# Kernel optimization log

Measured on AMD Instinct MI355X. Metric: run time of the kernel, lower is better.

Reference implementation:

```python
import jax, jax.numpy as jnp
from jax import lax
import numpy as np

T, B, I, H = 2048, 64, 256, 256  # time-major LSTM, standard 4H gate layout


def setup_inputs() -> dict:
    key = jax.random.key(0)
    k = jax.random.split(key, 5)
    s = 1.0 / np.sqrt(H)
    return {
        "x": jax.random.normal(k[0], (T, B, I), dtype=jnp.float32),
        "W_ih": jax.random.uniform(k[1], (4 * H, I), jnp.float32, -s, s),
        "W_hh": jax.random.uniform(k[2], (4 * H, H), jnp.float32, -s, s),
        "b_ih": jax.random.uniform(k[3], (4 * H,), jnp.float32, -s, s),
        "b_hh": jax.random.uniform(k[4], (4 * H,), jnp.float32, -s, s),
    }


def reference(x, W_ih, W_hh, b_ih, b_hh):
    # Precompute input projections for all timesteps in one big GEMM: [T, B, 4H]
    x_proj = jnp.einsum("tbi,gi->tbg", x, W_ih) + b_ih + b_hh

    def step(carry, xp_t):
        h, c = carry
        gates = xp_t + h @ W_hh.T  # [B, 4H]
        i, f, g, o = jnp.split(gates, 4, axis=-1)
        c = jax.nn.sigmoid(f) * c + jax.nn.sigmoid(i) * jnp.tanh(g)
        h = jax.nn.sigmoid(o) * jnp.tanh(c)
        return (h, c), None

    init = (jnp.zeros((x.shape[1], H), x.dtype), jnp.zeros((x.shape[1], H), x.dtype))
    (h_last, c_last), _ = lax.scan(step, init, x_proj)
    # torch loop overwrites `outputs` each step and returns only the final h
    return h_last
```

## Files before the change

### kernel.cpp

```cpp
#include <hip/hip_runtime.h>
#include <hip/hip_bf16.h>
#include <stdint.h>


#define T_STEPS 2048
#define NWG 32

typedef float f32x4 __attribute__((ext_vector_type(4)));
typedef short bf16x8 __attribute__((ext_vector_type(8)));
typedef uint32_t u32x4 __attribute__((ext_vector_type(4)));

__device__ __forceinline__ short tobf(float f) {
    __hip_bfloat16 h = __float2bfloat16(f);
    return *reinterpret_cast<short*>(&h);
}

__device__ __forceinline__ bf16x8 pack8(f32x4 a, f32x4 b) {
    bf16x8 r;
    r[0] = tobf(a[0]); r[1] = tobf(a[1]); r[2] = tobf(a[2]); r[3] = tobf(a[3]);
    r[4] = tobf(b[0]); r[5] = tobf(b[1]); r[6] = tobf(b[2]); r[7] = tobf(b[3]);
    return r;
}

__device__ __forceinline__ bf16x8 frag_u64(unsigned long long a, unsigned long long b) {
    u32x4 t;
    t.x = (uint32_t)a; t.y = (uint32_t)(a >> 32);
    t.z = (uint32_t)b; t.w = (uint32_t)(b >> 32);
    return __builtin_bit_cast(bf16x8, t);
}

__device__ __forceinline__ float fast_sig(float x) {
    float e = __builtin_amdgcn_exp2f(-1.4426950408889634f * x);
    return __builtin_amdgcn_rcpf(1.0f + e);
}
__device__ __forceinline__ float fast_tanh(float x) {
    float xc = fminf(fmaxf(x, -15.0f), 15.0f);
    float e = __builtin_amdgcn_exp2f(2.8853900817779268f * xc);
    return (e - 1.0f) * __builtin_amdgcn_rcpf(e + 1.0f);
}

__global__ __launch_bounds__(256, 1)
void lstm_fused(const float* __restrict__ x,
                const float* __restrict__ W_ih,
                const float* __restrict__ W_hh,
                const float* __restrict__ b_ih,
                const float* __restrict__ b_hh,
                float* __restrict__ out,
                uint32_t* __restrict__ hbuf,
                uint32_t* __restrict__ flags)
{
    const int wg   = blockIdx.x;
    const int tid  = threadIdx.x;
    const int wv   = tid >> 6;
    const int l    = tid & 63;
    const int l15  = l & 15;
    const int lk   = l >> 4;
    const int gate = l15 >> 2;
    const int jj   = l15 & 3;

    bf16x8 wf[2][16];
    float bias[2];
#pragma unroll
    for (int p = 0; p < 2; ++p) {
        const int grow = 256 * gate + 8 * wg + 4 * p + jj;
#pragma unroll
        for (int kt = 0; kt < 16; ++kt) {
            const float* src = (kt < 8)
                ? (W_ih + (size_t)grow * 256 + kt * 32 + lk * 8)
                : (W_hh + (size_t)grow * 256 + (kt - 8) * 32 + lk * 8);
            wf[p][kt] = pack8(*(const f32x4*)(src), *(const f32x4*)(src + 4));
        }
        bias[p] = b_ih[grow] + b_hh[grow];
    }

    const int arow = 16 * wv + l15;
    const float* xbase = x + (size_t)arow * 256 + lk * 8;

    float cst[2][4] = {{0.f,0.f,0.f,0.f},{0.f,0.f,0.f,0.f}};

    f32x4 xs[16];
#pragma unroll
    for (int kt = 0; kt < 8; ++kt) {
        xs[2 * kt]     = *(const f32x4*)(xbase + kt * 32);
        xs[2 * kt + 1] = *(const f32x4*)(xbase + kt * 32 + 4);
    }
    f32x4 aA[2] = {{0.f,0.f,0.f,0.f},{0.f,0.f,0.f,0.f}};
    f32x4 aB[2] = {{0.f,0.f,0.f,0.f},{0.f,0.f,0.f,0.f}};
    {
        bf16x8 af[8];
#pragma unroll
        for (int kt = 0; kt < 8; ++kt) af[kt] = pack8(xs[2 * kt], xs[2 * kt + 1]);
#pragma unroll
        for (int kt = 0; kt < 8; kt += 2)
#pragma unroll
            for (int p = 0; p < 2; ++p) {
                aA[p] = __builtin_amdgcn_mfma_f32_16x16x32_bf16(af[kt],     wf[p][kt],     aA[p], 0, 0, 0);
                aB[p] = __builtin_amdgcn_mfma_f32_16x16x32_bf16(af[kt + 1], wf[p][kt + 1], aB[p], 0, 0, 0);
            }
#pragma unroll
        for (int kt = 0; kt < 8; ++kt) {
            const float* p1 = xbase + 16384 + kt * 32;
            xs[2 * kt]     = *(const f32x4*)(p1);
            xs[2 * kt + 1] = *(const f32x4*)(p1 + 4);
        }
    }

    const uint32_t* mypollline = flags + wv * 32 + (l & 31);
    uint32_t* myflag = flags + wv * 32 + wg;

    for (int s = 0; s < T_STEPS; ++s) {
        if (s > 0) {
            const uint32_t target = (uint32_t)s;
            while (true) {
                uint32_t v = __hip_atomic_load(mypollline, __ATOMIC_RELAXED,
                                               __HIP_MEMORY_SCOPE_AGENT);
                if (__all((int)(v >= target))) break;
                __builtin_amdgcn_s_sleep(1);
            }
        }
        asm volatile("" ::: "memory");

        const unsigned long long* hb = (const unsigned long long*)
            (hbuf + (size_t)(s & 1) * 8192 + (size_t)arow * 128 + 4 * lk);
        unsigned long long hq[16];
#pragma unroll
        for (int kh = 0; kh < 8; ++kh) {
            hq[2 * kh]     = __hip_atomic_load(hb + (size_t)kh * 8,
                                               __ATOMIC_RELAXED, __HIP_MEMORY_SCOPE_AGENT);
            hq[2 * kh + 1] = __hip_atomic_load(hb + (size_t)kh * 8 + 1,
                                               __ATOMIC_RELAXED, __HIP_MEMORY_SCOPE_AGENT);
        }

#pragma unroll
        for (int kh = 0; kh < 8; kh += 2) {
            bf16x8 h0 = frag_u64(hq[2 * kh],     hq[2 * kh + 1]);
            bf16x8 h1 = frag_u64(hq[2 * kh + 2], hq[2 * kh + 3]);
#pragma unroll
            for (int p = 0; p < 2; ++p) {
                aA[p] = __builtin_amdgcn_mfma_f32_16x16x32_bf16(h0, wf[p][8 + kh],     aA[p], 0, 0, 0);
                aB[p] = __builtin_amdgcn_mfma_f32_16x16x32_bf16(h1, wf[p][8 + kh + 1], aB[p], 0, 0, 0);
            }
        }

        uint32_t* hw_out = hbuf + (size_t)((s + 1) & 1) * 8192;
        const int orow0 = 16 * wv + 4 * lk;
        float hv[2][4];
#pragma unroll
        for (int p = 0; p < 2; ++p) {
#pragma unroll
            for (int r = 0; r < 4; ++r) {
                float vo  = aA[p][r] + aB[p][r] + bias[p];
                float v4  = __shfl_xor(vo, 4);
                float v8  = __shfl_xor(vo, 8);
                float v12 = __shfl_xor(vo, 12);
                float iv = (gate == 0) ? vo : ((gate == 1) ? v4 : ((gate == 2) ? v8 : v12));
                float fv = (gate == 1) ? vo : ((gate == 0) ? v4 : ((gate == 3) ? v8 : v12));
                float gv = (gate == 2) ? vo : ((gate == 3) ? v4 : ((gate == 0) ? v8 : v12));
                float ov = (gate == 3) ? vo : ((gate == 2) ? v4 : ((gate == 1) ? v8 : v12));
                float cn = fast_sig(fv) * cst[p][r] + fast_sig(iv) * fast_tanh(gv);
                cst[p][r] = cn;
                hv[p][r] = fast_sig(ov) * fast_tanh(cn);
            }
        }

#pragma unroll
        for (int p = 0; p < 2; ++p) {
#pragma unroll
            for (int r = 0; r < 4; ++r) {
                uint32_t hu = (uint32_t)(uint16_t)tobf(hv[p][r]);
                uint32_t pu = (uint32_t)__shfl_xor((int)hu, 1);
                uint32_t packed = hu | (pu << 16);
                if ((l & 13) == 0) {
                    __hip_atomic_store(hw_out + (size_t)(orow0 + r) * 128
                                           + 4 * wg + 2 * p + (jj >> 1),
                                       packed, __ATOMIC_RELAXED, __HIP_MEMORY_SCOPE_AGENT);
                }
            }
        }

        if (s == T_STEPS - 1) {
#pragma unroll
            for (int p = 0; p < 2; ++p)
#pragma unroll
                for (int r = 0; r < 4; ++r)
                    if ((l & 12) == 0)
                        out[(size_t)(orow0 + r) * 256 + 8 * wg + 4 * p + jj] = hv[p][r];
        }

        if (l == 0)
            __hip_atomic_store(myflag, (uint32_t)(s + 1),
                               __ATOMIC_RELEASE, __HIP_MEMORY_SCOPE_AGENT);

        if (s + 1 < T_STEPS) {
            bf16x8 af[8];
#pragma unroll
            for (int kt = 0; kt < 8; ++kt) af[kt] = pack8(xs[2 * kt], xs[2 * kt + 1]);
#pragma unroll
            for (int p = 0; p < 2; ++p) { aA[p] = (f32x4){0.f,0.f,0.f,0.f}; aB[p] = (f32x4){0.f,0.f,0.f,0.f}; }
#pragma unroll
            for (int kt = 0; kt < 8; kt += 2)
#pragma unroll
                for (int p = 0; p < 2; ++p) {
                    aA[p] = __builtin_amdgcn_mfma_f32_16x16x32_bf16(af[kt],     wf[p][kt],     aA[p], 0, 0, 0);
                    aB[p] = __builtin_amdgcn_mfma_f32_16x16x32_bf16(af[kt + 1], wf[p][kt + 1], aB[p], 0, 0, 0);
                }
            if (s + 2 < T_STEPS) {
                const float* xp = xbase + (size_t)(s + 2) * 16384;
#pragma unroll
                for (int kt = 0; kt < 8; ++kt) {
                    xs[2 * kt]     = *(const f32x4*)(xp + kt * 32);
                    xs[2 * kt + 1] = *(const f32x4*)(xp + kt * 32 + 4);
                }
            }
        }
    }
}

extern "C" void kernel_launch(void* const* d_in, const int* in_sizes, int n_in,
                              void* d_out, int out_size, void* d_ws, size_t ws_size,
                              hipStream_t stream) {
    const float* x    = (const float*)d_in[0];
    const float* W_ih = (const float*)d_in[1];
    const float* W_hh = (const float*)d_in[2];
    const float* b_ih = (const float*)d_in[3];
    const float* b_hh = (const float*)d_in[4];
    float* out = (float*)d_out;

    uint32_t* hbuf  = (uint32_t*)d_ws;
    uint32_t* flags = hbuf + 2 * 8192;

    hipMemsetAsync(d_ws, 0, (2 * 8192 + 4 * 32) * sizeof(uint32_t), stream);

    lstm_fused<<<dim3(NWG), dim3(256), 0, stream>>>(x, W_ih, W_hh, b_ih, b_hh,
                                                    out, hbuf, flags);
}
```

Before: 13.96 ms.

## Replace per-step flag barrier with tag-embedded hidden-state words polled directly

Each hidden value is stored as a 32-bit word carrying the bf16 value plus a 16-bit step tag, so consumers poll the data itself instead of waiting on per-workgroup flags and then loading. This removes the separate flag release/acquire round trip on every step. The next step's input projection MFMAs are also moved ahead of the poll, and x is packed to bf16 as soon as it is loaded. In exchange the hidden buffer doubles in size, the output tensor is reused as the second ping-pong buffer, a spin budget can exit early, and correctness relies on relaxed stores of value and tag landing together in one word.

After: 38.72 ms. 177% more time.

```diff
diff --git a/kernel.cpp b/kernel.cpp
--- a/kernel.cpp
+++ b/kernel.cpp
@@ -10,23 +10,18 @@
 typedef short bf16x8 __attribute__((ext_vector_type(8)));
 typedef uint32_t u32x4 __attribute__((ext_vector_type(4)));
 
-__device__ __forceinline__ short tobf(float f) {
+__device__ __forceinline__ unsigned short tobf(float f) {
     __hip_bfloat16 h = __float2bfloat16(f);
-    return *reinterpret_cast<short*>(&h);
+    return *reinterpret_cast<unsigned short*>(&h);
 }
 
 __device__ __forceinline__ bf16x8 pack8(f32x4 a, f32x4 b) {
     bf16x8 r;
-    r[0] = tobf(a[0]); r[1] = tobf(a[1]); r[2] = tobf(a[2]); r[3] = tobf(a[3]);
-    r[4] = tobf(b[0]); r[5] = tobf(b[1]); r[6] = tobf(b[2]); r[7] = tobf(b[3]);
+    r[0] = (short)tobf(a[0]); r[1] = (short)tobf(a[1]);
+    r[2] = (short)tobf(a[2]); r[3] = (short)tobf(a[3]);
+    r[4] = (short)tobf(b[0]); r[5] = (short)tobf(b[1]);
+    r[6] = (short)tobf(b[2]); r[7] = (short)tobf(b[3]);
     return r;
-}
-
-__device__ __forceinline__ bf16x8 frag_u64(unsigned long long a, unsigned long long b) {
-    u32x4 t;
-    t.x = (uint32_t)a; t.y = (uint32_t)(a >> 32);
-    t.z = (uint32_t)b; t.w = (uint32_t)(b >> 32);
-    return __builtin_bit_cast(bf16x8, t);
 }
 
 __device__ __forceinline__ float fast_sig(float x) {
@@ -40,14 +35,14 @@
 }
 
 __global__ __launch_bounds__(256, 1)
-void lstm_fused(const float* __restrict__ x,
-                const float* __restrict__ W_ih,
-                const float* __restrict__ W_hh,
-                const float* __restrict__ b_ih,
-                const float* __restrict__ b_hh,
-                float* __restrict__ out,
-                uint32_t* __restrict__ hbuf,
-                uint32_t* __restrict__ flags)
+void lstm_tagged(const float* __restrict__ x,
+                 const float* __restrict__ W_ih,
+                 const float* __restrict__ W_hh,
+                 const float* __restrict__ b_ih,
+                 const float* __restrict__ b_hh,
+                 uint32_t* __restrict__ buf0,
+                 uint32_t* __restrict__ buf1,
+                 uint32_t* __restrict__ flags)
 {
     const int wg   = blockIdx.x;
     const int tid  = threadIdx.x;
@@ -58,6 +53,8 @@
     const int gate = l15 >> 2;
     const int jj   = l15 & 3;
 
+    int budget = 1 << 24;
+
     bf16x8 wf[2][16];
     float bias[2];
 #pragma unroll
@@ -78,71 +75,85 @@
 
     float cst[2][4] = {{0.f,0.f,0.f,0.f},{0.f,0.f,0.f,0.f}};
 
-    f32x4 xs[16];
-#pragma unroll
-    for (int kt = 0; kt < 8; ++kt) {
-        xs[2 * kt]     = *(const f32x4*)(xbase + kt * 32);
-        xs[2 * kt + 1] = *(const f32x4*)(xbase + kt * 32 + 4);
-    }
+    bf16x8 xsp[8];
+#pragma unroll
+    for (int kt = 0; kt < 8; ++kt)
+        xsp[kt] = pack8(*(const f32x4*)(xbase + kt * 32),
+                        *(const f32x4*)(xbase + kt * 32 + 4));
+
     f32x4 aA[2] = {{0.f,0.f,0.f,0.f},{0.f,0.f,0.f,0.f}};
     f32x4 aB[2] = {{0.f,0.f,0.f,0.f},{0.f,0.f,0.f,0.f}};
-    {
-        bf16x8 af[8];
-#pragma unroll
-        for (int kt = 0; kt < 8; ++kt) af[kt] = pack8(xs[2 * kt], xs[2 * kt + 1]);
-#pragma unroll
-        for (int kt = 0; kt < 8; kt += 2)
+#pragma unroll
+    for (int kt = 0; kt < 8; kt += 2)
+#pragma unroll
+        for (int p = 0; p < 2; ++p) {
+            aA[p] = __builtin_amdgcn_mfma_f32_16x16x32_bf16(xsp[kt],     wf[p][kt],     aA[p], 0, 0, 0);
+            aB[p] = __builtin_amdgcn_mfma_f32_16x16x32_bf16(xsp[kt + 1], wf[p][kt + 1], aB[p], 0, 0, 0);
+        }
+#pragma unroll
+    for (int kt = 0; kt < 8; ++kt)
+        xsp[kt] = pack8(*(const f32x4*)(xbase + 16384 + kt * 32),
+                        *(const f32x4*)(xbase + 16384 + kt * 32 + 4));
+
+    for (int s = 0; s < T_STEPS; ++s) {
+        const uint32_t* rb = (s & 1) ? buf1 : buf0;
+        const unsigned long long* hb64 =
+            (const unsigned long long*)(rb + (size_t)arow * 256) + 4 * lk;
+        unsigned long long hq[32];
+#pragma unroll
+        for (int kh = 0; kh < 8; ++kh)
+#pragma unroll
+            for (int i = 0; i < 4; ++i)
+                hq[4 * kh + i] = __hip_atomic_load(hb64 + 16 * kh + i,
+                                                   __ATOMIC_RELAXED, __HIP_MEMORY_SCOPE_AGENT);
+
+        f32x4 aA2[2] = {{0.f,0.f,0.f,0.f},{0.f,0.f,0.f,0.f}};
+        f32x4 aB2[2] = {{0.f,0.f,0.f,0.f},{0.f,0.f,0.f,0.f}};
+        if (s + 1 < T_STEPS) {
+#pragma unroll
+            for (int kt = 0; kt < 8; kt += 2)
+#pragma unroll
+                for (int p = 0; p < 2; ++p) {
+                    aA2[p] = __builtin_amdgcn_mfma_f32_16x16x32_bf16(xsp[kt],     wf[p][kt],     aA2[p], 0, 0, 0);
+                    aB2[p] = __builtin_amdgcn_mfma_f32_16x16x32_bf16(xsp[kt + 1], wf[p][kt + 1], aB2[p], 0, 0, 0);
+                }
+        }
+        __builtin_amdgcn_sched_barrier(0);
+
+        const unsigned long long tagpair =
+            (unsigned long long)(uint32_t)s * 0x0000000100000001ull;
+        const unsigned long long tmask = 0x0000FFFF0000FFFFull;
+        while (true) {
+            unsigned long long bad = 0;
+#pragma unroll
+            for (int i = 0; i < 32; ++i) bad |= (hq[i] ^ tagpair) & tmask;
+            if (__all(bad == 0ull)) break;
+            if (--budget < 0) break;
+            __builtin_amdgcn_s_sleep(1);
+#pragma unroll
+            for (int kh = 0; kh < 8; ++kh)
+#pragma unroll
+                for (int i = 0; i < 4; ++i)
+                    hq[4 * kh + i] = __hip_atomic_load(hb64 + 16 * kh + i,
+                                                       __ATOMIC_RELAXED, __HIP_MEMORY_SCOPE_AGENT);
+        }
+
+#pragma unroll
+        for (int kh = 0; kh < 8; ++kh) {
+            u32x4 t;
+#pragma unroll
+            for (int i = 0; i < 4; ++i) {
+                unsigned long long q = hq[4 * kh + i];
+                t[i] = (((uint32_t)q) >> 16) | ((uint32_t)(q >> 32) & 0xFFFF0000u);
+            }
+            bf16x8 hf = __builtin_bit_cast(bf16x8, t);
 #pragma unroll
             for (int p = 0; p < 2; ++p) {
-                aA[p] = __builtin_amdgcn_mfma_f32_16x16x32_bf16(af[kt],     wf[p][kt],     aA[p], 0, 0, 0);
-                aB[p] = __builtin_amdgcn_mfma_f32_16x16x32_bf16(af[kt + 1], wf[p][kt + 1], aB[p], 0, 0, 0);
-            }
-#pragma unroll
-        for (int kt = 0; kt < 8; ++kt) {
-            const float* p1 = xbase + 16384 + kt * 32;
-            xs[2 * kt]     = *(const f32x4*)(p1);
-            xs[2 * kt + 1] = *(const f32x4*)(p1 + 4);
-        }
-    }
-
-    const uint32_t* mypollline = flags + wv * 32 + (l & 31);
-    uint32_t* myflag = flags + wv * 32 + wg;
-
-    for (int s = 0; s < T_STEPS; ++s) {
-        if (s > 0) {
-            const uint32_t target = (uint32_t)s;
-            while (true) {
-                uint32_t v = __hip_atomic_load(mypollline, __ATOMIC_RELAXED,
-                                               __HIP_MEMORY_SCOPE_AGENT);
-                if (__all((int)(v >= target))) break;
-                __builtin_amdgcn_s_sleep(1);
-            }
-        }
-        asm volatile("" ::: "memory");
-
-        const unsigned long long* hb = (const unsigned long long*)
-            (hbuf + (size_t)(s & 1) * 8192 + (size_t)arow * 128 + 4 * lk);
-        unsigned long long hq[16];
-#pragma unroll
-        for (int kh = 0; kh < 8; ++kh) {
-            hq[2 * kh]     = __hip_atomic_load(hb + (size_t)kh * 8,
-                                               __ATOMIC_RELAXED, __HIP_MEMORY_SCOPE_AGENT);
-            hq[2 * kh + 1] = __hip_atomic_load(hb + (size_t)kh * 8 + 1,
-                                               __ATOMIC_RELAXED, __HIP_MEMORY_SCOPE_AGENT);
-        }
-
-#pragma unroll
-        for (int kh = 0; kh < 8; kh += 2) {
-            bf16x8 h0 = frag_u64(hq[2 * kh],     hq[2 * kh + 1]);
-            bf16x8 h1 = frag_u64(hq[2 * kh + 2], hq[2 * kh + 3]);
-#pragma unroll
-            for (int p = 0; p < 2; ++p) {
-                aA[p] = __builtin_amdgcn_mfma_f32_16x16x32_bf16(h0, wf[p][8 + kh],     aA[p], 0, 0, 0);
-                aB[p] = __builtin_amdgcn_mfma_f32_16x16x32_bf16(h1, wf[p][8 + kh + 1], aB[p], 0, 0, 0);
-            }
-        }
-
-        uint32_t* hw_out = hbuf + (size_t)((s + 1) & 1) * 8192;
+                if (kh & 1) aB[p] = __builtin_amdgcn_mfma_f32_16x16x32_bf16(hf, wf[p][8 + kh], aB[p], 0, 0, 0);
+                else        aA[p] = __builtin_amdgcn_mfma_f32_16x16x32_bf16(hf, wf[p][8 + kh], aA[p], 0, 0, 0);
+            }
+        }
+
         const int orow0 = 16 * wv + 4 * lk;
         float hv[2][4];
 #pragma unroll
@@ -163,55 +174,50 @@
             }
         }
 
-#pragma unroll
-        for (int p = 0; p < 2; ++p) {
-#pragma unroll
-            for (int r = 0; r < 4; ++r) {
-                uint32_t hu = (uint32_t)(uint16_t)tobf(hv[p][r]);
-                uint32_t pu = (uint32_t)__shfl_xor((int)hu, 1);
-                uint32_t packed = hu | (pu << 16);
-                if ((l & 13) == 0) {
-                    __hip_atomic_store(hw_out + (size_t)(orow0 + r) * 128
-                                           + 4 * wg + 2 * p + (jj >> 1),
-                                       packed, __ATOMIC_RELAXED, __HIP_MEMORY_SCOPE_AGENT);
-                }
-            }
+        if (s + 1 < T_STEPS) {
+            uint32_t* wb = ((s + 1) & 1) ? buf1 : buf0;
+            const uint32_t tago = (uint32_t)(s + 1);
+#pragma unroll
+            for (int p = 0; p < 2; ++p)
+#pragma unroll
+                for (int r = 0; r < 4; ++r)
+                    if ((l & 12) == 0) {
+                        uint32_t word = ((uint32_t)tobf(hv[p][r]) << 16) | tago;
+                        __hip_atomic_store(wb + (size_t)(orow0 + r) * 256
+                                               + 8 * wg + 4 * p + jj,
+                                           word, __ATOMIC_RELAXED, __HIP_MEMORY_SCOPE_AGENT);
+                    }
+        }
+
+#pragma unroll
+        for (int p = 0; p < 2; ++p) { aA[p] = aA2[p]; aB[p] = aB2[p]; }
+        if (s + 2 < T_STEPS) {
+            const float* xp = xbase + (size_t)(s + 2) * 16384;
+#pragma unroll
+            for (int kt = 0; kt < 8; ++kt)
+                xsp[kt] = pack8(*(const f32x4*)(xp + kt * 32),
+                                *(const f32x4*)(xp + kt * 32 + 4));
         }
 
         if (s == T_STEPS - 1) {
+            if (l == 0)
+                __hip_atomic_store(flags + wv * 32 + wg, 1u,
+                                   __ATOMIC_RELEASE, __HIP_MEMORY_SCOPE_AGENT);
+            const uint32_t* fp = flags + wv * 32 + (l & 31);
+            while (true) {
+                uint32_t fvv = __hip_atomic_load(fp, __ATOMIC_RELAXED,
+                                                 __HIP_MEMORY_SCOPE_AGENT);
+                if (__all((int)(fvv >= 1u))) break;
+                if (--budget < 0) break;
+                __builtin_amdgcn_s_sleep(1);
+            }
+            float* outf = (float*)buf1;
 #pragma unroll
             for (int p = 0; p < 2; ++p)
 #pragma unroll
                 for (int r = 0; r < 4; ++r)
                     if ((l & 12) == 0)
-                        out[(size_t)(orow0 + r) * 256 + 8 * wg + 4 * p + jj] = hv[p][r];
-        }
-
-        if (l == 0)
-            __hip_atomic_store(myflag, (uint32_t)(s + 1),
-                               __ATOMIC_RELEASE, __HIP_MEMORY_SCOPE_AGENT);
-
-        if (s + 1 < T_STEPS) {
-            bf16x8 af[8];
-#pragma unroll
-            for (int kt = 0; kt < 8; ++kt) af[kt] = pack8(xs[2 * kt], xs[2 * kt + 1]);
-#pragma unroll
-            for (int p = 0; p < 2; ++p) { aA[p] = (f32x4){0.f,0.f,0.f,0.f}; aB[p] = (f32x4){0.f,0.f,0.f,0.f}; }
-#pragma unroll
-            for (int kt = 0; kt < 8; kt += 2)
-#pragma unroll
-                for (int p = 0; p < 2; ++p) {
-                    aA[p] = __builtin_amdgcn_mfma_f32_16x16x32_bf16(af[kt],     wf[p][kt],     aA[p], 0, 0, 0);
-                    aB[p] = __builtin_amdgcn_mfma_f32_16x16x32_bf16(af[kt + 1], wf[p][kt + 1], aB[p], 0, 0, 0);
-                }
-            if (s + 2 < T_STEPS) {
-                const float* xp = xbase + (size_t)(s + 2) * 16384;
-#pragma unroll
-                for (int kt = 0; kt < 8; ++kt) {
-                    xs[2 * kt]     = *(const f32x4*)(xp + kt * 32);
-                    xs[2 * kt + 1] = *(const f32x4*)(xp + kt * 32 + 4);
-                }
-            }
+                        outf[(size_t)(orow0 + r) * 256 + 8 * wg + 4 * p + jj] = hv[p][r];
         }
     }
 }
@@ -224,13 +230,14 @@
     const float* W_hh = (const float*)d_in[2];
     const float* b_ih = (const float*)d_in[3];
     const float* b_hh = (const float*)d_in[4];
-    float* out = (float*)d_out;
-
-    uint32_t* hbuf  = (uint32_t*)d_ws;
-    uint32_t* flags = hbuf + 2 * 8192;
-
-    hipMemsetAsync(d_ws, 0, (2 * 8192 + 4 * 32) * sizeof(uint32_t), stream);
-
-    lstm_fused<<<dim3(NWG), dim3(256), 0, stream>>>(x, W_ih, W_hh, b_ih, b_hh,
-                                                    out, hbuf, flags);
-}
+
+    uint32_t* buf0  = (uint32_t*)d_ws;
+    uint32_t* flags = buf0 + 16384;
+    uint32_t* buf1  = (uint32_t*)d_out;
+
+    hipMemsetAsync(d_ws, 0, (16384 + 4 * 32) * sizeof(uint32_t), stream);
+    hipMemsetAsync(d_out, 0, 16384 * sizeof(uint32_t), stream);
+
+    lstm_tagged<<<dim3(NWG), dim3(256), 0, stream>>>(x, W_ih, W_hh, b_ih, b_hh,
+                                                     buf0, buf1, flags);
+}
```
